# Optimization experiments

Hardware: AMD Instinct MI355X
Metric: run time of the kernel (lower is better)

Reference implementation:

```python
import jax, jax.numpy as jnp
import numpy as np

B, E, S, H = 8, 1024, 2048, 16  # batch, embed_dim, seq_len, n_heads
D = E // H                       # per-head hidden dim


def setup_inputs() -> dict:
    key = jax.random.key(0)
    k1, k2 = jax.random.split(key)
    x = jax.random.normal(k1, (B, E, S), dtype=jnp.float32)
    weight = jax.random.normal(k2, (H, S), dtype=jnp.float32)  # nn.Parameter(torch.randn)
    bias = jnp.zeros((H, S), dtype=jnp.float32)                # nn.Parameter(torch.zeros)
    return {"x": x, "weight": weight, "bias": bias}


def _vector_to_matrix(v):
    # v: (H, S) -> M: (H, S, S), M[h, i, j] = v[h, j - i] if j >= i else 0
    h, m = v.shape
    i = jnp.arange(m)[:, None]
    j = jnp.arange(m)[None, :]
    off = j - i  # negative offsets wrap (same as torch fancy indexing) but are masked out
    return jnp.where(j >= i, v[:, off], jnp.zeros((), dtype=v.dtype))


def reference(x, weight, bias):
    b, e, s = x.shape
    h = weight.shape[0]
    d = e // h
    M = _vector_to_matrix(weight)  # (H, S, S)
    # Original: x.view(B,H,D,S).reshape(B*H,D,S) paired with W.repeat_interleave(B,0),
    # i.e. flat index k uses M[k // B]. Group the flat B*H axis into H contiguous
    # blocks of size B so each block shares one Toeplitz matrix (no (B*H,S,S) blowup).
    xg = x.reshape(b * h, d, s).reshape(h, b, d, s)  # block m = M[m]
    out = jnp.einsum('mbds,mst->mbdt', xg, M) + bias[:, None, None, :]
    return out.reshape(b, e, s)
```

## Files before the change

### kernel.cpp

```cpp
#include <hip/hip_runtime.h>
#include <hip/hip_bf16.h>

#define SEQ    2048
#define NHEAD  16
#define RPH    512
#define BM     128
#define BK     64
#define NTH    256

#define WSTRIDE 2184
#define ABUF_E  8192
#define WCOP_E  (2 * ABUF_E)
#define TOT_E   (WCOP_E + 8 * WSTRIDE)

typedef float  f32x4  __attribute__((ext_vector_type(4)));
typedef __bf16 bf16x8 __attribute__((ext_vector_type(8)));

struct PF { float4 v0, v1, v2, v3, v4, v5, v6, v7; };

__device__ __forceinline__ unsigned f2bf(float f) {
    union { __hip_bfloat16 h; unsigned short u; } cv;
    cv.h = __float2bfloat16(f);
    return (unsigned)cv.u;
}

__device__ __forceinline__ uint4 pack8u(float4 a, float4 b) {
    union { bf16x8 v; uint4 u; } r;
    r.v[0] = (__bf16)a.x; r.v[1] = (__bf16)a.y;
    r.v[2] = (__bf16)a.z; r.v[3] = (__bf16)a.w;
    r.v[4] = (__bf16)b.x; r.v[5] = (__bf16)b.y;
    r.v[6] = (__bf16)b.z; r.v[7] = (__bf16)b.w;
    return r.u;
}

#define MFMA16(a, b, c) __builtin_amdgcn_mfma_f32_16x16x32_bf16((a), (b), (c), 0, 0, 0)

#define LOADPF(P, CH)                                                         \
  { const float* g_ = Xp + (size_t)(CH) * BK;                                 \
    P.v0 = *(const float4*)g_;                                                \
    P.v1 = *(const float4*)(g_ + 4);                                          \
    P.v2 = *(const float4*)(g_ + 8 * SEQ);                                    \
    P.v3 = *(const float4*)(g_ + 8 * SEQ + 4);                                \
    P.v4 = *(const float4*)(g_ + 16 * SEQ);                                   \
    P.v5 = *(const float4*)(g_ + 16 * SEQ + 4);                               \
    P.v6 = *(const float4*)(g_ + 24 * SEQ);                                   \
    P.v7 = *(const float4*)(g_ + 24 * SEQ + 4); }

#define WRITEA(AB, P)                                                         \
  { *(uint4*)((AB) + wb0) = pack8u(P.v0, P.v1);                               \
    *(uint4*)((AB) + wb1) = pack8u(P.v2, P.v3);                               \
    *(uint4*)((AB) + wb2) = pack8u(P.v4, P.v5);                               \
    *(uint4*)((AB) + wb3) = pack8u(P.v6, P.v7); }

#define BODY(ABC, ABN, PFW, PFL, CH)                                          \
  {                                                                           \
    if ((CH) + 2 < nch) LOADPF(PFL, (CH) + 2);                                \
    if ((CH) + 1 < nch) WRITEA(ABN, PFW);                                     \
    const int s0_ = (CH) * BK;                                                \
    __builtin_amdgcn_s_setprio(1);                                            \
    _Pragma("unroll")                                                         \
    for (int ks = 0; ks < 2; ++ks) {                                          \
      const int kb_ = (64 * ks + kq16) ^ swz;                                 \
      bf16x8 af0 = *(const bf16x8*)((ABC) + Arow0 + kb_);                     \
      bf16x8 af1 = *(const bf16x8*)((ABC) + Arow1 + kb_);                     \
      const unsigned short* bp_ = wc + (Bc0 + s0_ + 32 * ks - 112);           \
      bf16x8 bf0 = *(const bf16x8*)(bp_ + 112);                               \
      bf16x8 bf1 = *(const bf16x8*)(bp_ + 96);                                \
      bf16x8 bf2 = *(const bf16x8*)(bp_ + 80);                                \
      bf16x8 bf3 = *(const bf16x8*)(bp_ + 64);                                \
      bf16x8 bf4 = *(const bf16x8*)(bp_ + 48);                                \
      bf16x8 bf5 = *(const bf16x8*)(bp_ + 32);                                \
      bf16x8 bf6 = *(const bf16x8*)(bp_ + 16);                                \
      bf16x8 bf7 = *(const bf16x8*)(bp_);                                     \
      acc[0][0] = MFMA16(af0, bf0, acc[0][0]);                                \
      acc[1][0] = MFMA16(af1, bf0, acc[1][0]);                                \
      acc[0][1] = MFMA16(af0, bf1, acc[0][1]);                                \
      acc[1][1] = MFMA16(af1, bf1, acc[1][1]);                                \
      acc[0][2] = MFMA16(af0, bf2, acc[0][2]);                                \
      acc[1][2] = MFMA16(af1, bf2, acc[1][2]);                                \
      acc[0][3] = MFMA16(af0, bf3, acc[0][3]);                                \
      acc[1][3] = MFMA16(af1, bf3, acc[1][3]);                                \
      acc[0][4] = MFMA16(af0, bf4, acc[0][4]);                                \
      acc[1][4] = MFMA16(af1, bf4, acc[1][4]);                                \
      acc[0][5] = MFMA16(af0, bf5, acc[0][5]);                                \
      acc[1][5] = MFMA16(af1, bf5, acc[1][5]);                                \
      acc[0][6] = MFMA16(af0, bf6, acc[0][6]);                                \
      acc[1][6] = MFMA16(af1, bf6, acc[1][6]);                                \
      acc[0][7] = MFMA16(af0, bf7, acc[0][7]);                                \
      acc[1][7] = MFMA16(af1, bf7, acc[1][7]);                                \
    }                                                                         \
    __builtin_amdgcn_s_setprio(0);                                            \
  }

__global__ __launch_bounds__(NTH, 2) void mixer_kernel(
    const float* __restrict__ x, const float* __restrict__ wgt,
    const float* __restrict__ bias, float* __restrict__ out)
{
    __shared__ unsigned short smem[TOT_E] __attribute__((aligned(16)));
    char* ab0 = (char*)smem;
    char* ab1 = (char*)smem + ABUF_E * 2;
    unsigned short* wc = smem + WCOP_E;

    const int tid  = threadIdx.x;
    const int lane = tid & 63;
    const int wv   = tid >> 6;

    const int bid  = blockIdx.x;
    const int m    = (bid & 7) + 8 * ((bid >> 3) & 1);
    const int rt   = (bid >> 4) & 3;
    const int pr   = bid >> 6;
    const int ct_hi = 15 - pr;
    const int ct_lo = pr;

    const float* Xb = x   + (size_t)(m * RPH + rt * BM) * SEQ;
    float*       Ob = out + (size_t)(m * RPH + rt * BM) * SEQ;
    const float* wr = wgt  + m * SEQ;
    const float* br = bias + m * SEQ;

    const int sr    = lane >> 3;
    const int sc    = (lane & 7) * 8;
    const int wsw   = ((lane & 7) * 16) ^ (sr << 4);
    const int rbw   = 32 * wv;
    const int wb0   = (rbw + sr)      * 128 + wsw;
    const int wb1   = (rbw + sr + 8)  * 128 + wsw;
    const int wb2   = (rbw + sr + 16) * 128 + wsw;
    const int wb3   = (rbw + sr + 24) * 128 + wsw;
    const float* Xp = Xb + (size_t)(rbw + sr) * SEQ + sc;

    PF pfA, pfB;
    LOADPF(pfA, 0);
    LOADPF(pfB, 1);

    {
        const int t8 = tid * 8;
        const float* g = wr + (2040 - t8);
        float4 lo = *(const float4*)g;
        float4 hi = *(const float4*)(g + 4);
        uint4 v;
        v.x = f2bf(hi.w) | (f2bf(hi.z) << 16);
        v.y = f2bf(hi.y) | (f2bf(hi.x) << 16);
        v.z = f2bf(lo.w) | (f2bf(lo.z) << 16);
        v.w = f2bf(lo.y) | (f2bf(lo.x) << 16);
        *(uint4*)(smem + 8 + t8) = v;
        if (tid < 21) {
            uint4 z = {0u, 0u, 0u, 0u};
            unsigned short* dst = (tid == 0) ? smem
                                 : smem + 8 + 2048 + (tid - 1) * 8;
            *(uint4*)dst = z;
        }
    }
    __syncthreads();

    #pragma unroll
    for (int c = 0; c < 8; ++c) {
        for (int grp = tid; grp < WSTRIDE / 8; grp += NTH) {
            const int i = grp * 8;
            uint4 g0 = *(const uint4*)(smem + 8 + i - 8);
            uint4 g1 = *(const uint4*)(smem + 8 + i);
            unsigned d[9] = {g0.x, g0.y, g0.z, g0.w,
                             g1.x, g1.y, g1.z, g1.w, 0u};
            const int qd = (16 - 2 * c) >> 2;
            uint4 o;
            if (c & 1) {
                o.x = (d[qd]     >> 16) | (d[qd + 1] << 16);
                o.y = (d[qd + 1] >> 16) | (d[qd + 2] << 16);
                o.z = (d[qd + 2] >> 16) | (d[qd + 3] << 16);
                o.w = (d[qd + 3] >> 16) | (d[qd + 4] << 16);
            } else {
                o.x = d[qd];     o.y = d[qd + 1];
                o.z = d[qd + 2]; o.w = d[qd + 3];
            }
            *(uint4*)(wc + c * WSTRIDE + i) = o;
        }
    }
    __syncthreads();

    const int col_low = lane & 15;
    const int kq      = lane >> 4;
    const int kq16    = kq * 16;
    const int swz     = (col_low & 7) << 4;
    const int cpy     = (col_low + 1) & 7;
    const int BcBase  = cpy * WSTRIDE + cpy + 2047 - col_low + 8 * kq;
    const int Arow0   = (rbw      + col_low) * 128;
    const int Arow1   = (rbw + 16 + col_low) * 128;

    #pragma unroll
    for (int half = 0; half < 2; ++half) {
        const int ct  = half ? ct_lo : ct_hi;
        const int t0  = ct << 7;
        const int nch = 2 * (ct + 1);
        const int Bc0 = BcBase - t0;

        if (half) { LOADPF(pfA, 0); LOADPF(pfB, 1); }
        WRITEA(ab0, pfA);

        f32x4 acc[2][8] = {};
        for (int ch = 0; ch < nch; ch += 2) {
            BODY(ab0, ab1, pfB, pfA, ch);
            BODY(ab1, ab0, pfA, pfB, ch + 1);
        }

        #pragma unroll
        for (int c = 0; c < 8; ++c) {
            const int colg = t0 + 16 * c + col_low;
            const float bv = br[colg];
            #pragma unroll
            for (int a = 0; a < 2; ++a) {
                const int rowl = rbw + 16 * a + 4 * kq;
                #pragma unroll
                for (int r = 0; r < 4; ++r)
                    __builtin_nontemporal_store(acc[a][c][r] + bv,
                        Ob + (size_t)(rowl + r) * SEQ + colg);
            }
        }
    }
}

extern "C" void kernel_launch(void* const* d_in, const int* in_sizes, int n_in,
                              void* d_out, int out_size, void* d_ws, size_t ws_size,
                              hipStream_t stream) {
    const float* x  = (const float*)d_in[0];
    const float* w  = (const float*)d_in[1];
    const float* bs = (const float*)d_in[2];
    float* out = (float*)d_out;
    dim3 grid(512);
    dim3 block(NTH);
    hipLaunchKernelGGL(mixer_kernel, grid, block, 0, stream, x, w, bs, out);
}
```

Before: 49.43 us.

## Shrink K-chunk to 32, rotate Toeplitz B fragments in registers, raise occupancy

Halves the K chunk per pipeline stage to 32, which halves the A staging buffers and the prefetch registers. Because B is a Toeplitz matrix, consecutive column fragments are shifted copies of each other, so most of them are now kept in a rotating register window and only two new fragments are loaded from LDS per chunk. The smaller LDS and register footprint lets launch bounds ask for three blocks per CU instead of two. It also drops the LDS A swizzle and replaces the nontemporal output stores with plain stores, which may bring LDS bank conflicts and more cache pollution.

```diff
diff --git a/kernel.cpp b/kernel.cpp
--- a/kernel.cpp
+++ b/kernel.cpp
@@ -5,18 +5,18 @@
 #define NHEAD  16
 #define RPH    512
 #define BM     128
-#define BK     64
+#define BK     32
 #define NTH    256
 
 #define WSTRIDE 2184
-#define ABUF_E  8192
-#define WCOP_E  (2 * ABUF_E)
+#define ABUF_B  8192
+#define WCOP_E  8192
 #define TOT_E   (WCOP_E + 8 * WSTRIDE)
 
 typedef float  f32x4  __attribute__((ext_vector_type(4)));
 typedef __bf16 bf16x8 __attribute__((ext_vector_type(8)));
 
-struct PF { float4 v0, v1, v2, v3, v4, v5, v6, v7; };
+struct PF { float4 v0, v1, v2, v3; };
 
 __device__ __forceinline__ unsigned f2bf(float f) {
     union { __hip_bfloat16 h; unsigned short u; } cv;
@@ -35,70 +35,54 @@
 
 #define MFMA16(a, b, c) __builtin_amdgcn_mfma_f32_16x16x32_bf16((a), (b), (c), 0, 0, 0)
 
-#define LOADPF(P, CH)                                                         \
-  { const float* g_ = Xp + (size_t)(CH) * BK;                                 \
+#define LOADPF(P, OFF)                                                        \
+  { const float* g_ = Xt + (OFF);                                             \
     P.v0 = *(const float4*)g_;                                                \
     P.v1 = *(const float4*)(g_ + 4);                                          \
-    P.v2 = *(const float4*)(g_ + 8 * SEQ);                                    \
-    P.v3 = *(const float4*)(g_ + 8 * SEQ + 4);                                \
-    P.v4 = *(const float4*)(g_ + 16 * SEQ);                                   \
-    P.v5 = *(const float4*)(g_ + 16 * SEQ + 4);                               \
-    P.v6 = *(const float4*)(g_ + 24 * SEQ);                                   \
-    P.v7 = *(const float4*)(g_ + 24 * SEQ + 4); }
+    P.v2 = *(const float4*)(g_ + 16 * SEQ);                                   \
+    P.v3 = *(const float4*)(g_ + 16 * SEQ + 4); }
 
 #define WRITEA(AB, P)                                                         \
   { *(uint4*)((AB) + wb0) = pack8u(P.v0, P.v1);                               \
-    *(uint4*)((AB) + wb1) = pack8u(P.v2, P.v3);                               \
-    *(uint4*)((AB) + wb2) = pack8u(P.v4, P.v5);                               \
-    *(uint4*)((AB) + wb3) = pack8u(P.v6, P.v7); }
-
-#define BODY(ABC, ABN, PFW, PFL, CH)                                          \
+    *(uint4*)((AB) + wb1) = pack8u(P.v2, P.v3); }
+
+#define CHUNK32(J, ABC, ABN, PFN, LAST)                                       \
   {                                                                           \
-    if ((CH) + 2 < nch) LOADPF(PFL, (CH) + 2);                                \
-    if ((CH) + 1 < nch) WRITEA(ABN, PFW);                                     \
-    const int s0_ = (CH) * BK;                                                \
+    if (!(LAST) || (J) < 3) WRITEA(ABN, PFN);                                 \
+    if (!(LAST) || (J) < 1) LOADPF(PFN, 32 * (J) + 96);                       \
     __builtin_amdgcn_s_setprio(1);                                            \
-    _Pragma("unroll")                                                         \
-    for (int ks = 0; ks < 2; ++ks) {                                          \
-      const int kb_ = (64 * ks + kq16) ^ swz;                                 \
-      bf16x8 af0 = *(const bf16x8*)((ABC) + Arow0 + kb_);                     \
-      bf16x8 af1 = *(const bf16x8*)((ABC) + Arow1 + kb_);                     \
-      const unsigned short* bp_ = wc + (Bc0 + s0_ + 32 * ks - 112);           \
-      bf16x8 bf0 = *(const bf16x8*)(bp_ + 112);                               \
-      bf16x8 bf1 = *(const bf16x8*)(bp_ + 96);                                \
-      bf16x8 bf2 = *(const bf16x8*)(bp_ + 80);                                \
-      bf16x8 bf3 = *(const bf16x8*)(bp_ + 64);                                \
-      bf16x8 bf4 = *(const bf16x8*)(bp_ + 48);                                \
-      bf16x8 bf5 = *(const bf16x8*)(bp_ + 32);                                \
-      bf16x8 bf6 = *(const bf16x8*)(bp_ + 16);                                \
-      bf16x8 bf7 = *(const bf16x8*)(bp_);                                     \
-      acc[0][0] = MFMA16(af0, bf0, acc[0][0]);                                \
-      acc[1][0] = MFMA16(af1, bf0, acc[1][0]);                                \
-      acc[0][1] = MFMA16(af0, bf1, acc[0][1]);                                \
-      acc[1][1] = MFMA16(af1, bf1, acc[1][1]);                                \
-      acc[0][2] = MFMA16(af0, bf2, acc[0][2]);                                \
-      acc[1][2] = MFMA16(af1, bf2, acc[1][2]);                                \
-      acc[0][3] = MFMA16(af0, bf3, acc[0][3]);                                \
-      acc[1][3] = MFMA16(af1, bf3, acc[1][3]);                                \
-      acc[0][4] = MFMA16(af0, bf4, acc[0][4]);                                \
-      acc[1][4] = MFMA16(af1, bf4, acc[1][4]);                                \
-      acc[0][5] = MFMA16(af0, bf5, acc[0][5]);                                \
-      acc[1][5] = MFMA16(af1, bf5, acc[1][5]);                                \
-      acc[0][6] = MFMA16(af0, bf6, acc[0][6]);                                \
-      acc[1][6] = MFMA16(af1, bf6, acc[1][6]);                                \
-      acc[0][7] = MFMA16(af0, bf7, acc[0][7]);                                \
-      acc[1][7] = MFMA16(af1, bf7, acc[1][7]);                                \
+    bf16x8 af0 = *(const bf16x8*)((ABC) + Arow0 + kq16);                      \
+    bf16x8 af1 = *(const bf16x8*)((ABC) + Arow1 + kq16);                      \
+    acc[0][0] = MFMA16(af0, bwc[(2*(J)+8)&7], acc[0][0]);                     \
+    acc[1][0] = MFMA16(af1, bwc[(2*(J)+8)&7], acc[1][0]);                     \
+    acc[0][1] = MFMA16(af0, bwc[(2*(J)+7)&7], acc[0][1]);                     \
+    acc[1][1] = MFMA16(af1, bwc[(2*(J)+7)&7], acc[1][1]);                     \
+    acc[0][2] = MFMA16(af0, bwc[(2*(J)+6)&7], acc[0][2]);                     \
+    acc[1][2] = MFMA16(af1, bwc[(2*(J)+6)&7], acc[1][2]);                     \
+    acc[0][3] = MFMA16(af0, bwc[(2*(J)+5)&7], acc[0][3]);                     \
+    acc[1][3] = MFMA16(af1, bwc[(2*(J)+5)&7], acc[1][3]);                     \
+    acc[0][4] = MFMA16(af0, bwc[(2*(J)+4)&7], acc[0][4]);                     \
+    acc[1][4] = MFMA16(af1, bwc[(2*(J)+4)&7], acc[1][4]);                     \
+    acc[0][5] = MFMA16(af0, bwc[(2*(J)+3)&7], acc[0][5]);                     \
+    acc[1][5] = MFMA16(af1, bwc[(2*(J)+3)&7], acc[1][5]);                     \
+    acc[0][6] = MFMA16(af0, bwc[(2*(J)+2)&7], acc[0][6]);                     \
+    acc[1][6] = MFMA16(af1, bwc[(2*(J)+2)&7], acc[1][6]);                     \
+    acc[0][7] = MFMA16(af0, bwc[(2*(J)+1)&7], acc[0][7]);                     \
+    acc[1][7] = MFMA16(af1, bwc[(2*(J)+1)&7], acc[1][7]);                     \
+    __builtin_amdgcn_s_setprio(0);                                            \
+    if (!(LAST) || (J) < 3) {                                                 \
+      bwc[(2*(J)+1)&7] = *(const bf16x8*)(wp + 32*(J) + 16);                  \
+      bwc[(2*(J)+2)&7] = *(const bf16x8*)(wp + 32*(J) + 32);                  \
     }                                                                         \
-    __builtin_amdgcn_s_setprio(0);                                            \
   }
 
-__global__ __launch_bounds__(NTH, 2) void mixer_kernel(
+__global__ __launch_bounds__(NTH, 3) void mixer_kernel(
     const float* __restrict__ x, const float* __restrict__ wgt,
     const float* __restrict__ bias, float* __restrict__ out)
 {
     __shared__ unsigned short smem[TOT_E] __attribute__((aligned(16)));
     char* ab0 = (char*)smem;
-    char* ab1 = (char*)smem + ABUF_E * 2;
+    char* ab1 = (char*)smem + ABUF_B;
     unsigned short* wc = smem + WCOP_E;
 
     const int tid  = threadIdx.x;
@@ -117,19 +101,15 @@
     const float* wr = wgt  + m * SEQ;
     const float* br = bias + m * SEQ;
 
-    const int sr    = lane >> 3;
-    const int sc    = (lane & 7) * 8;
-    const int wsw   = ((lane & 7) * 16) ^ (sr << 4);
+    const int sr2   = lane >> 2;
+    const int sc2   = (lane & 3) * 8;
     const int rbw   = 32 * wv;
-    const int wb0   = (rbw + sr)      * 128 + wsw;
-    const int wb1   = (rbw + sr + 8)  * 128 + wsw;
-    const int wb2   = (rbw + sr + 16) * 128 + wsw;
-    const int wb3   = (rbw + sr + 24) * 128 + wsw;
-    const float* Xp = Xb + (size_t)(rbw + sr) * SEQ + sc;
-
-    PF pfA, pfB;
-    LOADPF(pfA, 0);
-    LOADPF(pfB, 1);
+    const int wb0   = (rbw + sr2) * 64 + (lane & 3) * 16;
+    const int wb1   = wb0 + 1024;
+    const float* Xp = Xb + (size_t)(rbw + sr2) * SEQ + sc2;
+
+    PF pf0, pf1;
+    { const float* Xt = Xp; LOADPF(pf0, 0); LOADPF(pf1, 32); }
 
     {
         const int t8 = tid * 8;
@@ -178,27 +158,46 @@
     const int col_low = lane & 15;
     const int kq      = lane >> 4;
     const int kq16    = kq * 16;
-    const int swz     = (col_low & 7) << 4;
     const int cpy     = (col_low + 1) & 7;
     const int BcBase  = cpy * WSTRIDE + cpy + 2047 - col_low + 8 * kq;
-    const int Arow0   = (rbw      + col_low) * 128;
-    const int Arow1   = (rbw + 16 + col_low) * 128;
-
-    #pragma unroll
+    const int Arow0   = (rbw + col_low) * 64;
+    const int Arow1   = Arow0 + 1024;
+
     for (int half = 0; half < 2; ++half) {
         const int ct  = half ? ct_lo : ct_hi;
         const int t0  = ct << 7;
-        const int nch = 2 * (ct + 1);
-        const int Bc0 = BcBase - t0;
-
-        if (half) { LOADPF(pfA, 0); LOADPF(pfB, 1); }
-        WRITEA(ab0, pfA);
+        const int nch = 4 * (ct + 1);
+        const unsigned short* wp = wc + (BcBase - t0);
+        const float* Xt = Xp;
+
+        if (half) { LOADPF(pf0, 0); LOADPF(pf1, 32); }
+        WRITEA(ab0, pf0);
+        LOADPF(pf0, 64);
+
+        bf16x8 bwc[8];
+        bwc[0] = *(const bf16x8*)(wp);
+        bwc[7] = *(const bf16x8*)(wp - 16);
+        bwc[6] = *(const bf16x8*)(wp - 32);
+        bwc[5] = *(const bf16x8*)(wp - 48);
+        bwc[4] = *(const bf16x8*)(wp - 64);
+        bwc[3] = *(const bf16x8*)(wp - 80);
+        bwc[2] = *(const bf16x8*)(wp - 96);
+        bwc[1] = *(const bf16x8*)(wp - 112);
 
         f32x4 acc[2][8] = {};
-        for (int ch = 0; ch < nch; ch += 2) {
-            BODY(ab0, ab1, pfB, pfA, ch);
-            BODY(ab1, ab0, pfA, pfB, ch + 1);
-        }
+        const int nt1 = (nch >> 2) - 1;
+        for (int t = 0; t < nt1; ++t) {
+            CHUNK32(0, ab0, ab1, pf1, 0);
+            CHUNK32(1, ab1, ab0, pf0, 0);
+            CHUNK32(2, ab0, ab1, pf1, 0);
+            CHUNK32(3, ab1, ab0, pf0, 0);
+            Xt += 4 * BK;
+            wp += 4 * BK;
+        }
+        CHUNK32(0, ab0, ab1, pf1, 1);
+        CHUNK32(1, ab1, ab0, pf0, 1);
+        CHUNK32(2, ab0, ab1, pf1, 1);
+        CHUNK32(3, ab1, ab0, pf0, 1);
 
         #pragma unroll
         for (int c = 0; c < 8; ++c) {
@@ -209,8 +208,7 @@
                 const int rowl = rbw + 16 * a + 4 * kq;
                 #pragma unroll
                 for (int r = 0; r < 4; ++r)
-                    __builtin_nontemporal_store(acc[a][c][r] + bv,
-                        Ob + (size_t)(rowl + r) * SEQ + colg);
+                    Ob[(size_t)(rowl + r) * SEQ + colg] = acc[a][c][r] + bv;
             }
         }
     }
```

New measurement: 50.90 us. 3.0% more time.
